# Kernel optimization log

Hardware: AMD Instinct MI355X
Metric: run time of the kernel (lower is better)

## Reference

```python
import jax, jax.numpy as jnp
import numpy as np

B, T, DQ, DV, A, F, K = 64, 1024, 1024, 512, 512, 32, 31


def setup_inputs() -> dict:
    key = jax.random.key(0)
    ks = jax.random.split(key, 8)
    query = jax.random.normal(ks[0], (B, DQ), jnp.float32)
    values = jax.random.normal(ks[1], (B, T, DV), jnp.float32)
    # decoder-step states (as produced by init_states)
    attention_cum = jnp.zeros((B, T), jnp.float32)
    attention_old = jnp.zeros((B, T), jnp.float32)
    alpha = jnp.concatenate([jnp.ones((B, 1), jnp.float32),
                             jnp.zeros((B, T - 1), jnp.float32) + 1e-7], axis=1)
    # learned parameters (Glorot-ish scaling)
    W_query = jax.random.normal(ks[2], (DQ, A), jnp.float32) / np.sqrt(DQ)
    W_inputs = jax.random.normal(ks[3], (DV, A), jnp.float32) / np.sqrt(DV)
    v_w = jax.random.normal(ks[4], (A, 1), jnp.float32) / np.sqrt(A)
    v_b = jnp.zeros((1,), jnp.float32)
    loc_kernel = jax.random.normal(ks[5], (K, 2, F), jnp.float32) / np.sqrt(K * 2)  # WIO
    W_loc = jax.random.normal(ks[6], (F, A), jnp.float32) / np.sqrt(F)
    return {"query": query, "values": values, "attention_cum": attention_cum,
            "attention_old": attention_old, "alpha": alpha,
            "W_query": W_query, "W_inputs": W_inputs, "v_w": v_w, "v_b": v_b,
            "loc_kernel": loc_kernel, "W_loc": W_loc}


def reference(query, values, attention_cum, attention_old, alpha,
              W_query, W_inputs, v_w, v_b, loc_kernel, W_loc):
    # process_values: cached projection of encoder memory  [B,T,A]
    processed_values = jnp.einsum('btd,da->bta', values, W_inputs)
    # location features: conv over stacked (old, cum) attention  [B,T,2]->[B,T,F]
    attn_cat = jnp.stack([attention_old, attention_cum], axis=2)
    conv = jax.lax.conv_general_dilated(attn_cat, loc_kernel, window_strides=(1,),
                                        padding='SAME',
                                        dimension_numbers=('NWC', 'WIO', 'NWC'))
    processed_attn = jnp.einsum('btf,fa->bta', conv, W_loc)
    # query projection  [B,1,A]
    processed_query = (query @ W_query)[:, None, :]
    # additive score  [B,T]
    score = (jnp.tanh(processed_values + processed_query + processed_attn) @ v_w)[..., 0] + v_b
    scores_norm = jax.nn.softmax(score, axis=-1)
    # forward attention recursion
    fwd_shifted = jnp.pad(alpha[:, :-1], ((0, 0), (1, 0)))
    new_alpha = (0.5 * alpha + 0.5 * fwd_shifted + 1e-8) * scores_norm
    new_alpha = new_alpha / jnp.sum(new_alpha, axis=1, keepdims=True)
    attn_weights = new_alpha
    # updated states
    new_cum = attention_cum + scores_norm
    new_old = attn_weights
    # context vector  [B,DV]
    context = jnp.einsum('bt,btd->bd', attn_weights, values)
    return (context, attn_weights, new_cum, new_old, new_alpha)
```

## Files before the change

### kernel.cpp

```cpp
#include <hip/hip_runtime.h>
#include <hip/hip_bf16.h>
#include <cstdint>
#include <cstddef>

#define B 64
#define T 1024
#define DQ 1024
#define DV 512
#define A_DIM 512
#define F_DIM 32
#define KW 31
#define M_TOT (B*T)
#define KEXT2 576
#define NCH 9

typedef __attribute__((ext_vector_type(8))) short short8;
typedef __attribute__((ext_vector_type(4))) float f32x4;
typedef __attribute__((ext_vector_type(4))) unsigned u32x4;

static __device__ __forceinline__ unsigned short f2bf(float f) {
    unsigned int u = __builtin_bit_cast(unsigned int, f);
    u += 0x7fffu + ((u >> 16) & 1u);
    return (unsigned short)(u >> 16);
}
static __device__ __forceinline__ float tanh_fast(float x) {
    float e = __expf(2.0f * x);
    return 1.0f - 2.0f * __builtin_amdgcn_rcpf(e + 1.0f);
}
static __device__ __forceinline__ short8 cvt8(f32x4 a, f32x4 b) {
    unsigned u0, u1, u2, u3;
    asm("v_cvt_pk_bf16_f32 %0, %1, %2" : "=v"(u0) : "v"(a[0]), "v"(a[1]));
    asm("v_cvt_pk_bf16_f32 %0, %1, %2" : "=v"(u1) : "v"(a[2]), "v"(a[3]));
    asm("v_cvt_pk_bf16_f32 %0, %1, %2" : "=v"(u2) : "v"(b[0]), "v"(b[1]));
    asm("v_cvt_pk_bf16_f32 %0, %1, %2" : "=v"(u3) : "v"(b[2]), "v"(b[3]));
    u32x4 u; u[0] = u0; u[1] = u1; u[2] = u2; u[3] = u3;
    return __builtin_bit_cast(short8, u);
}

#define LDSDMA16(gptr, lptr)                                                        \
    __builtin_amdgcn_global_load_lds(                                               \
        (const __attribute__((address_space(1))) void*)(const void*)(gptr),         \
        (__attribute__((address_space(3))) void*)(void*)(lptr), 16, 0, 0)

__global__ void prep_kernel(const float* __restrict__ query, const float* __restrict__ Wq,
                            const float* __restrict__ Wi, const float* __restrict__ Wl,
                            const float* __restrict__ old_, const float* __restrict__ cum_,
                            const float* __restrict__ lk,
                            float* __restrict__ pq,
                            float* __restrict__ score, unsigned short* __restrict__ Bt,
                            unsigned short* __restrict__ convb) {
    __shared__ __align__(16) char smem[16640];
    int bid = blockIdx.x, tid = threadIdx.x;
    if (bid < 512) {
        float (*red)[64] = (float(*)[64])smem;
        int pid = bid;
        int gid = pid * 256 + tid;
        if (gid < M_TOT) score[gid] = 0.f;
        int b = pid >> 3, a0 = (pid & 7) * 64;
        int al = tid & 63, ks = tid >> 6;
        const float* qr = query + (size_t)b * DQ + ks * 256;
        const float* wc = Wq + (size_t)(ks * 256) * A_DIM + a0 + al;
        float acc = 0.f;
        #pragma unroll 8
        for (int k = 0; k < 256; ++k) acc += qr[k] * wc[(size_t)k * A_DIM];
        red[ks][al] = acc;
        __syncthreads();
        if (ks == 0)
            pq[b * A_DIM + a0 + al] = red[0][al] + red[1][al] + red[2][al] + red[3][al];
    } else if (bid < 584) {
        float (*tile)[65] = (float(*)[65])smem;
        int tb = bid - 512;
        if (tb < 64) {
            int k0 = (tb >> 3) * 64, a0 = (tb & 7) * 64;
            int al = tid & 63, ko = tid >> 6;
            #pragma unroll
            for (int j = 0; j < 16; ++j) {
                int kl = j * 4 + ko;
                tile[kl][al] = Wi[(size_t)(k0 + kl) * A_DIM + a0 + al];
            }
            __syncthreads();
            int kl2 = tid & 63, ao = tid >> 6;
            #pragma unroll
            for (int j = 0; j < 16; ++j) {
                int al2 = j * 4 + ao;
                Bt[(size_t)(a0 + al2) * KEXT2 + k0 + kl2] = f2bf(tile[kl2][al2]);
            }
        } else {
            int a0 = (tb - 64) * 64;
            int al = tid & 63, ko = tid >> 6;
            #pragma unroll
            for (int j = 0; j < 8; ++j) {
                int kl = j * 4 + ko;
                tile[kl][al] = Wl[(size_t)kl * A_DIM + a0 + al];
            }
            __syncthreads();
            int kl2 = tid & 31, ao = tid >> 5;
            #pragma unroll
            for (int j = 0; j < 8; ++j) {
                int al2 = j * 8 + ao;
                Bt[(size_t)(a0 + al2) * KEXT2 + DV + kl2] = f2bf(tile[kl2][al2]);
            }
            #pragma unroll
            for (int j = 0; j < 8; ++j) {
                int idx = j * 256 + tid;
                int a_l = idx >> 5, kp = idx & 31;
                Bt[(size_t)(a0 + a_l) * KEXT2 + 544 + kp] = 0;
            }
        }
    } else {
        float* sOld = (float*)smem;
        float* sCum = sOld + 94;
        float* sLK  = sCum + 94;
        int cid = bid - 584;
        int b = cid >> 4, t0 = (cid & 15) * 64;
        int tl = tid & 63, fg = tid >> 6;
        for (int j = tid; j < 94; j += 256) {
            int tt = t0 - 15 + j;
            bool ok = (tt >= 0 && tt < T);
            sOld[j] = ok ? old_[b * T + tt] : 0.f;
            sCum[j] = ok ? cum_[b * T + tt] : 0.f;
        }
        for (int j = tid; j < KW * 2 * F_DIM; j += 256) sLK[j] = lk[j];
        __syncthreads();
        float acc[8];
        #pragma unroll
        for (int f = 0; f < 8; ++f) acc[f] = 0.f;
        for (int k = 0; k < KW; ++k) {
            float o = sOld[tl + k], c = sCum[tl + k];
            const float* lo = &sLK[(k * 2 + 0) * F_DIM + fg * 8];
            const float* lc = &sLK[(k * 2 + 1) * F_DIM + fg * 8];
            #pragma unroll
            for (int f = 0; f < 8; ++f) acc[f] += o * lo[f] + c * lc[f];
        }
        short8 pk;
        #pragma unroll
        for (int f = 0; f < 8; ++f) pk[f] = (short)f2bf(acc[f]);
        unsigned short* dst = convb + (size_t)(b * T + t0 + tl) * 64 + fg * 8;
        *(short8*)dst = pk;
        *(short8*)(dst + 32) = (short8)0;
    }
}

__launch_bounds__(256, 3)
__global__ void gemm_score(const float* __restrict__ values,
                           const unsigned short* __restrict__ Bt,
                           const unsigned short* __restrict__ convb,
                           const float* __restrict__ pq,
                           const float* __restrict__ vw,
                           float* __restrict__ score) {
    __shared__ __align__(16) float sAf[128 * 64];
    __shared__ __align__(16) short sB[128 * 64];
    __shared__ float sPQ[128];
    __shared__ float sVW[128];
    int tid = threadIdx.x;
    int x = blockIdx.x & 7, l = blockIdx.x >> 3;
    int mt = x * 64 + (l >> 2), nq = l & 3;
    int m0 = mt * 128, n0 = nq * 128;
    int b = m0 >> 10;
    if (tid < 128) { sPQ[tid] = pq[b * A_DIM + n0 + tid]; sVW[tid] = vw[n0 + tid]; }
    int w = tid >> 6, lane = tid & 63, q = lane >> 4, l15 = lane & 15;
    int wm = w & 1, wn = w >> 1;
    int trow = tid >> 4, pA = tid & 15;
    const float* aBase = values + (size_t)(m0 + trow) * DV + (pA ^ trow) * 4;
    int brow = tid >> 3, bseg = ((tid & 7) - brow) & 7;
    const unsigned short* bBase = Bt + (size_t)(n0 + brow) * KEXT2 + bseg * 8;
    const unsigned short* cBase = convb + (size_t)(m0 + brow) * 64 + bseg * 8;

    f32x4 acc[4][4];
    #pragma unroll
    for (int mi = 0; mi < 4; ++mi)
        #pragma unroll
        for (int ni = 0; ni < 4; ++ni) acc[mi][ni] = (f32x4)0.f;

    for (int c = 0; c < NCH; ++c) {
        __syncthreads();
        if (c < 8) {
            #pragma unroll
            for (int j = 0; j < 8; ++j)
                LDSDMA16(aBase + (size_t)j * 16 * DV + c * 64,
                         &sAf[(j * 256 + w * 64) * 4]);
        } else {
            #pragma unroll
            for (int j = 0; j < 4; ++j)
                LDSDMA16(cBase + j * 32 * 64,
                         (short*)sAf + (j * 256 + w * 64) * 8);
        }
        #pragma unroll
        for (int j = 0; j < 4; ++j)
            LDSDMA16(bBase + (size_t)j * 32 * KEXT2 + c * 64,
                     &sB[(j * 256 + w * 64) * 8]);
        __syncthreads();
        #pragma unroll
        for (int h = 0; h < 2; ++h) {
            short8 af[4], bfr[4];
            #pragma unroll
            for (int ni = 0; ni < 4; ++ni) {
                int r = wn * 64 + ni * 16 + l15;
                bfr[ni] = *(const short8*)&sB[r * 64 + ((((h * 4 + q) + r) & 7) << 3)];
            }
            if (c < 8) {
                #pragma unroll
                for (int mi = 0; mi < 4; ++mi) {
                    int r = wm * 64 + mi * 16 + l15;
                    int ps = (h * 8 + q * 2) ^ l15;
                    f32x4 lo = *(const f32x4*)&sAf[r * 64 + ps * 4];
                    f32x4 hi = *(const f32x4*)&sAf[r * 64 + (ps ^ 1) * 4];
                    af[mi] = cvt8(lo, hi);
                }
            } else {
                const short* sAh = (const short*)sAf;
                #pragma unroll
                for (int mi = 0; mi < 4; ++mi) {
                    int r = wm * 64 + mi * 16 + l15;
                    af[mi] = *(const short8*)&sAh[r * 64 + ((((h * 4 + q) + r) & 7) << 3)];
                }
            }
            #pragma unroll
            for (int mi = 0; mi < 4; ++mi)
                #pragma unroll
                for (int ni = 0; ni < 4; ++ni)
                    acc[mi][ni] = __builtin_amdgcn_mfma_f32_16x16x32_bf16(af[mi], bfr[ni], acc[mi][ni], 0, 0, 0);
        }
    }
    #pragma unroll
    for (int mi = 0; mi < 4; ++mi) {
        #pragma unroll
        for (int r = 0; r < 4; ++r) {
            float s = 0.f;
            #pragma unroll
            for (int ni = 0; ni < 4; ++ni) {
                int col = wn * 64 + ni * 16 + l15;
                float xv = acc[mi][ni][r] + sPQ[col];
                s += tanh_fast(xv) * sVW[col];
            }
            #pragma unroll
            for (int off = 1; off < 16; off <<= 1) s += __shfl_xor(s, off, 64);
            if (l15 == 0)
                atomicAdd(&score[m0 + wm * 64 + mi * 16 + q * 4 + r], s);
        }
    }
}

__global__ void softmax_fwd(const float* __restrict__ score,
                            const float* __restrict__ alpha,
                            const float* __restrict__ cum,
                            float* __restrict__ out) {
    int b = blockIdx.x, t = threadIdx.x;
    __shared__ float sred[16];
    __shared__ float sbc;
    float sc = score[b * T + t];
    int wid = t >> 6, lane = t & 63;
    float m = sc;
    #pragma unroll
    for (int off = 32; off; off >>= 1) m = fmaxf(m, __shfl_xor(m, off, 64));
    if (lane == 0) sred[wid] = m;
    __syncthreads();
    if (t == 0) { float mm = sred[0]; for (int i = 1; i < 16; ++i) mm = fmaxf(mm, sred[i]); sbc = mm; }
    __syncthreads();
    float M = sbc;
    float e = __expf(sc - M);
    float s = e;
    #pragma unroll
    for (int off = 32; off; off >>= 1) s += __shfl_xor(s, off, 64);
    __syncthreads();
    if (lane == 0) sred[wid] = s;
    __syncthreads();
    if (t == 0) { float ss = 0.f; for (int i = 0; i < 16; ++i) ss += sred[i]; sbc = ss; }
    __syncthreads();
    float sn = e / sbc;
    float a_t = alpha[b * T + t];
    float a_p = (t > 0) ? alpha[b * T + t - 1] : 0.f;
    float ua = (0.5f * (a_t + a_p) + 1e-8f) * sn;
    float u = ua;
    #pragma unroll
    for (int off = 32; off; off >>= 1) u += __shfl_xor(u, off, 64);
    __syncthreads();
    if (lane == 0) sred[wid] = u;
    __syncthreads();
    if (t == 0) { float ss = 0.f; for (int i = 0; i < 16; ++i) ss += sred[i]; sbc = ss; }
    __syncthreads();
    float wgt = ua / sbc;
    float* attnw  = out + B * DV;
    float* ncum   = attnw + B * T;
    float* nold   = ncum + B * T;
    float* nalpha = nold + B * T;
    attnw[b * T + t]  = wgt;
    ncum[b * T + t]   = cum[b * T + t] + sn;
    nold[b * T + t]   = wgt;
    nalpha[b * T + t] = wgt;
    if (t < DV) out[b * DV + t] = 0.f;
}

__global__ void context_kernel(const float* __restrict__ values,
                               float* __restrict__ out) {
    __shared__ float red[4][256];
    const float* attnw = out + B * DV;
    int b = blockIdx.x >> 5, tq = (blockIdx.x >> 1) & 15, dh = blockIdx.x & 1;
    int sub = threadIdx.x >> 6, dg = threadIdx.x & 63;
    int t0 = tq * 64 + sub * 16;
    int d0 = dh * 256 + dg * 4;
    float acc[4];
    #pragma unroll
    for (int f = 0; f < 4; ++f) acc[f] = 0.f;
    for (int tt = 0; tt < 16; ++tt) {
        int t = t0 + tt;
        float wgt = attnw[b * T + t];
        float4 xv = *(const float4*)(values + (size_t)(b * T + t) * DV + d0);
        acc[0] += wgt * xv.x; acc[1] += wgt * xv.y;
        acc[2] += wgt * xv.z; acc[3] += wgt * xv.w;
    }
    #pragma unroll
    for (int f = 0; f < 4; ++f) red[sub][dg * 4 + f] = acc[f];
    __syncthreads();
    if (sub == 0) {
        #pragma unroll
        for (int f = 0; f < 4; ++f) {
            int di = dg * 4 + f;
            float s = red[0][di] + red[1][di] + red[2][di] + red[3][di];
            atomicAdd(&out[b * DV + dh * 256 + di], s);
        }
    }
}

extern "C" void kernel_launch(void* const* d_in, const int* in_sizes, int n_in,
                              void* d_out, int out_size, void* d_ws, size_t ws_size,
                              hipStream_t stream) {
    const float* query  = (const float*)d_in[0];
    const float* values = (const float*)d_in[1];
    const float* cum    = (const float*)d_in[2];
    const float* old_   = (const float*)d_in[3];
    const float* alpha  = (const float*)d_in[4];
    const float* Wq     = (const float*)d_in[5];
    const float* Wi     = (const float*)d_in[6];
    const float* vw     = (const float*)d_in[7];
    const float* lk     = (const float*)d_in[9];
    const float* Wl     = (const float*)d_in[10];
    float* out = (float*)d_out;
    char* ws = (char*)d_ws;
    float* ws_pq            = (float*)(ws);
    float* ws_score         = (float*)(ws + 131072);
    unsigned short* ws_Bt   = (unsigned short*)(ws + 393216);
    unsigned short* ws_conv = (unsigned short*)(ws + 1048576);

    prep_kernel<<<1608, 256, 0, stream>>>(query, Wq, Wi, Wl, old_, cum, lk,
                                          ws_pq, ws_score, ws_Bt, ws_conv);
    gemm_score<<<2048, 256, 0, stream>>>(values, ws_Bt, ws_conv, ws_pq, vw, ws_score);
    softmax_fwd<<<64, 1024, 0, stream>>>(ws_score, alpha, cum, out);
    context_kernel<<<2048, 256, 0, stream>>>(values, out);
}
```

Measured before the change: 295.9 us.

## Double-buffer LDS in gemm_score and widen N tile to 256

```diff
diff --git a/kernel.cpp b/kernel.cpp
--- a/kernel.cpp
+++ b/kernel.cpp
@@ -141,27 +141,27 @@
     }
 }
 
-__launch_bounds__(256, 3)
+__launch_bounds__(512, 1)
 __global__ void gemm_score(const float* __restrict__ values,
                            const unsigned short* __restrict__ Bt,
                            const unsigned short* __restrict__ convb,
                            const float* __restrict__ pq,
                            const float* __restrict__ vw,
                            float* __restrict__ score) {
-    __shared__ __align__(16) float sAf[128 * 64];
-    __shared__ __align__(16) short sB[128 * 64];
-    __shared__ float sPQ[128];
-    __shared__ float sVW[128];
+    __shared__ __align__(16) float sAf[2][128 * 64];
+    __shared__ __align__(16) short sB[2][256 * 64];
+    __shared__ float sPQ[256];
+    __shared__ float sVW[256];
     int tid = threadIdx.x;
     int x = blockIdx.x & 7, l = blockIdx.x >> 3;
-    int mt = x * 64 + (l >> 2), nq = l & 3;
-    int m0 = mt * 128, n0 = nq * 128;
+    int mt = x * 64 + (l >> 1), nq = l & 1;
+    int m0 = mt * 128, n0 = nq * 256;
     int b = m0 >> 10;
-    if (tid < 128) { sPQ[tid] = pq[b * A_DIM + n0 + tid]; sVW[tid] = vw[n0 + tid]; }
+    if (tid < 256) { sPQ[tid] = pq[b * A_DIM + n0 + tid]; sVW[tid] = vw[n0 + tid]; }
     int w = tid >> 6, lane = tid & 63, q = lane >> 4, l15 = lane & 15;
     int wm = w & 1, wn = w >> 1;
     int trow = tid >> 4, pA = tid & 15;
-    const float* aBase = values + (size_t)(m0 + trow) * DV + (pA ^ trow) * 4;
+    const float* aBase = values + (size_t)(m0 + trow) * DV + ((pA ^ (trow & 15)) * 4);
     int brow = tid >> 3, bseg = ((tid & 7) - brow) & 7;
     const unsigned short* bBase = Bt + (size_t)(n0 + brow) * KEXT2 + bseg * 8;
     const unsigned short* cBase = convb + (size_t)(m0 + brow) * 64 + bseg * 8;
@@ -172,43 +172,53 @@
         #pragma unroll
         for (int ni = 0; ni < 4; ++ni) acc[mi][ni] = (f32x4)0.f;
 
+    #pragma unroll
+    for (int j = 0; j < 4; ++j)
+        LDSDMA16(aBase + (size_t)j * 32 * DV, &sAf[0][(j * 512 + w * 64) * 4]);
+    #pragma unroll
+    for (int j = 0; j < 4; ++j)
+        LDSDMA16(bBase + (size_t)j * 64 * KEXT2, &sB[0][(j * 512 + w * 64) * 8]);
+    __syncthreads();
+
+    int cur = 0;
     for (int c = 0; c < NCH; ++c) {
-        __syncthreads();
-        if (c < 8) {
-            #pragma unroll
-            for (int j = 0; j < 8; ++j)
-                LDSDMA16(aBase + (size_t)j * 16 * DV + c * 64,
-                         &sAf[(j * 256 + w * 64) * 4]);
-        } else {
+        int nxt = cur ^ 1;
+        if (c + 1 < NCH) {
+            if (c + 1 < 8) {
+                #pragma unroll
+                for (int j = 0; j < 4; ++j)
+                    LDSDMA16(aBase + (size_t)j * 32 * DV + (c + 1) * 64,
+                             &sAf[nxt][(j * 512 + w * 64) * 4]);
+            } else {
+                #pragma unroll
+                for (int j = 0; j < 2; ++j)
+                    LDSDMA16(cBase + j * 64 * 64,
+                             (short*)&sAf[nxt][0] + (j * 512 + w * 64) * 8);
+            }
             #pragma unroll
             for (int j = 0; j < 4; ++j)
-                LDSDMA16(cBase + j * 32 * 64,
-                         (short*)sAf + (j * 256 + w * 64) * 8);
-        }
-        #pragma unroll
-        for (int j = 0; j < 4; ++j)
-            LDSDMA16(bBase + (size_t)j * 32 * KEXT2 + c * 64,
-                     &sB[(j * 256 + w * 64) * 8]);
-        __syncthreads();
+                LDSDMA16(bBase + (size_t)j * 64 * KEXT2 + (c + 1) * 64,
+                         &sB[nxt][(j * 512 + w * 64) * 8]);
+        }
         #pragma unroll
         for (int h = 0; h < 2; ++h) {
             short8 af[4], bfr[4];
             #pragma unroll
             for (int ni = 0; ni < 4; ++ni) {
                 int r = wn * 64 + ni * 16 + l15;
-                bfr[ni] = *(const short8*)&sB[r * 64 + ((((h * 4 + q) + r) & 7) << 3)];
+                bfr[ni] = *(const short8*)&sB[cur][r * 64 + ((((h * 4 + q) + r) & 7) << 3)];
             }
             if (c < 8) {
                 #pragma unroll
                 for (int mi = 0; mi < 4; ++mi) {
                     int r = wm * 64 + mi * 16 + l15;
                     int ps = (h * 8 + q * 2) ^ l15;
-                    f32x4 lo = *(const f32x4*)&sAf[r * 64 + ps * 4];
-                    f32x4 hi = *(const f32x4*)&sAf[r * 64 + (ps ^ 1) * 4];
+                    f32x4 lo = *(const f32x4*)&sAf[cur][r * 64 + ps * 4];
+                    f32x4 hi = *(const f32x4*)&sAf[cur][r * 64 + (ps ^ 1) * 4];
                     af[mi] = cvt8(lo, hi);
                 }
             } else {
-                const short* sAh = (const short*)sAf;
+                const short* sAh = (const short*)&sAf[cur][0];
                 #pragma unroll
                 for (int mi = 0; mi < 4; ++mi) {
                     int r = wm * 64 + mi * 16 + l15;
@@ -221,6 +231,8 @@
                 for (int ni = 0; ni < 4; ++ni)
                     acc[mi][ni] = __builtin_amdgcn_mfma_f32_16x16x32_bf16(af[mi], bfr[ni], acc[mi][ni], 0, 0, 0);
         }
+        __syncthreads();
+        cur = nxt;
     }
     #pragma unroll
     for (int mi = 0; mi < 4; ++mi) {
@@ -344,7 +356,7 @@
 
     prep_kernel<<<1608, 256, 0, stream>>>(query, Wq, Wi, Wl, old_, cum, lk,
                                           ws_pq, ws_score, ws_Bt, ws_conv);
-    gemm_score<<<2048, 256, 0, stream>>>(values, ws_Bt, ws_conv, ws_pq, vw, ws_score);
+    gemm_score<<<1024, 512, 0, stream>>>(values, ws_Bt, ws_conv, ws_pq, vw, ws_score);
     softmax_fwd<<<64, 1024, 0, stream>>>(ws_score, alpha, cum, out);
     context_kernel<<<2048, 256, 0, stream>>>(values, out);
 }
```

After: 318.6 us. +7.7%, slower.

## Load GEMM operands directly from global into registers, dropping LDS staging

Applied to the files above, without the earlier changes.

```diff
diff --git a/kernel.cpp b/kernel.cpp
--- a/kernel.cpp
+++ b/kernel.cpp
@@ -12,7 +12,6 @@
 #define KW 31
 #define M_TOT (B*T)
 #define KEXT2 576
-#define NCH 9
 
 typedef __attribute__((ext_vector_type(8))) short short8;
 typedef __attribute__((ext_vector_type(4))) float f32x4;
@@ -36,11 +35,6 @@
     u32x4 u; u[0] = u0; u[1] = u1; u[2] = u2; u[3] = u3;
     return __builtin_bit_cast(short8, u);
 }
-
-#define LDSDMA16(gptr, lptr)                                                        \
-    __builtin_amdgcn_global_load_lds(                                               \
-        (const __attribute__((address_space(1))) void*)(const void*)(gptr),         \
-        (__attribute__((address_space(3))) void*)(void*)(lptr), 16, 0, 0)
 
 __global__ void prep_kernel(const float* __restrict__ query, const float* __restrict__ Wq,
                             const float* __restrict__ Wi, const float* __restrict__ Wl,
@@ -148,23 +142,23 @@
                            const float* __restrict__ pq,
                            const float* __restrict__ vw,
                            float* __restrict__ score) {
-    __shared__ __align__(16) float sAf[128 * 64];
-    __shared__ __align__(16) short sB[128 * 64];
-    __shared__ float sPQ[128];
-    __shared__ float sVW[128];
     int tid = threadIdx.x;
     int x = blockIdx.x & 7, l = blockIdx.x >> 3;
     int mt = x * 64 + (l >> 2), nq = l & 3;
     int m0 = mt * 128, n0 = nq * 128;
     int b = m0 >> 10;
-    if (tid < 128) { sPQ[tid] = pq[b * A_DIM + n0 + tid]; sVW[tid] = vw[n0 + tid]; }
     int w = tid >> 6, lane = tid & 63, q = lane >> 4, l15 = lane & 15;
     int wm = w & 1, wn = w >> 1;
-    int trow = tid >> 4, pA = tid & 15;
-    const float* aBase = values + (size_t)(m0 + trow) * DV + (pA ^ trow) * 4;
-    int brow = tid >> 3, bseg = ((tid & 7) - brow) & 7;
-    const unsigned short* bBase = Bt + (size_t)(n0 + brow) * KEXT2 + bseg * 8;
-    const unsigned short* cBase = convb + (size_t)(m0 + brow) * 64 + bseg * 8;
+    int arow = m0 + wm * 64 + l15;
+    int bcol = n0 + wn * 64 + l15;
+    const float* aP0 = values + (size_t)(arow +  0) * DV + q * 8;
+    const float* aP1 = values + (size_t)(arow + 16) * DV + q * 8;
+    const float* aP2 = values + (size_t)(arow + 32) * DV + q * 8;
+    const float* aP3 = values + (size_t)(arow + 48) * DV + q * 8;
+    const unsigned short* bP0 = Bt + (size_t)(bcol +  0) * KEXT2 + q * 8;
+    const unsigned short* bP1 = Bt + (size_t)(bcol + 16) * KEXT2 + q * 8;
+    const unsigned short* bP2 = Bt + (size_t)(bcol + 32) * KEXT2 + q * 8;
+    const unsigned short* bP3 = Bt + (size_t)(bcol + 48) * KEXT2 + q * 8;
 
     f32x4 acc[4][4];
     #pragma unroll
@@ -172,55 +166,54 @@
         #pragma unroll
         for (int ni = 0; ni < 4; ++ni) acc[mi][ni] = (f32x4)0.f;
 
-    for (int c = 0; c < NCH; ++c) {
-        __syncthreads();
-        if (c < 8) {
-            #pragma unroll
-            for (int j = 0; j < 8; ++j)
-                LDSDMA16(aBase + (size_t)j * 16 * DV + c * 64,
-                         &sAf[(j * 256 + w * 64) * 4]);
-        } else {
-            #pragma unroll
-            for (int j = 0; j < 4; ++j)
-                LDSDMA16(cBase + j * 32 * 64,
-                         (short*)sAf + (j * 256 + w * 64) * 8);
-        }
-        #pragma unroll
-        for (int j = 0; j < 4; ++j)
-            LDSDMA16(bBase + (size_t)j * 32 * KEXT2 + c * 64,
-                     &sB[(j * 256 + w * 64) * 8]);
-        __syncthreads();
+    #pragma unroll 1
+    for (int c = 0; c < 8; ++c) {
         #pragma unroll
         for (int h = 0; h < 2; ++h) {
-            short8 af[4], bfr[4];
-            #pragma unroll
-            for (int ni = 0; ni < 4; ++ni) {
-                int r = wn * 64 + ni * 16 + l15;
-                bfr[ni] = *(const short8*)&sB[r * 64 + ((((h * 4 + q) + r) & 7) << 3)];
-            }
-            if (c < 8) {
-                #pragma unroll
-                for (int mi = 0; mi < 4; ++mi) {
-                    int r = wm * 64 + mi * 16 + l15;
-                    int ps = (h * 8 + q * 2) ^ l15;
-                    f32x4 lo = *(const f32x4*)&sAf[r * 64 + ps * 4];
-                    f32x4 hi = *(const f32x4*)&sAf[r * 64 + (ps ^ 1) * 4];
-                    af[mi] = cvt8(lo, hi);
-                }
-            } else {
-                const short* sAh = (const short*)sAf;
-                #pragma unroll
-                for (int mi = 0; mi < 4; ++mi) {
-                    int r = wm * 64 + mi * 16 + l15;
-                    af[mi] = *(const short8*)&sAh[r * 64 + ((((h * 4 + q) + r) & 7) << 3)];
-                }
-            }
+            f32x4 lo[4], hi[4];
+            short8 bfr[4], af[4];
+            lo[0] = *(const f32x4*)(aP0 + h * 32); hi[0] = *(const f32x4*)(aP0 + h * 32 + 4);
+            lo[1] = *(const f32x4*)(aP1 + h * 32); hi[1] = *(const f32x4*)(aP1 + h * 32 + 4);
+            lo[2] = *(const f32x4*)(aP2 + h * 32); hi[2] = *(const f32x4*)(aP2 + h * 32 + 4);
+            lo[3] = *(const f32x4*)(aP3 + h * 32); hi[3] = *(const f32x4*)(aP3 + h * 32 + 4);
+            bfr[0] = *(const short8*)(bP0 + h * 32);
+            bfr[1] = *(const short8*)(bP1 + h * 32);
+            bfr[2] = *(const short8*)(bP2 + h * 32);
+            bfr[3] = *(const short8*)(bP3 + h * 32);
+            #pragma unroll
+            for (int mi = 0; mi < 4; ++mi) af[mi] = cvt8(lo[mi], hi[mi]);
             #pragma unroll
             for (int mi = 0; mi < 4; ++mi)
                 #pragma unroll
                 for (int ni = 0; ni < 4; ++ni)
                     acc[mi][ni] = __builtin_amdgcn_mfma_f32_16x16x32_bf16(af[mi], bfr[ni], acc[mi][ni], 0, 0, 0);
         }
+        aP0 += 64; aP1 += 64; aP2 += 64; aP3 += 64;
+        bP0 += 64; bP1 += 64; bP2 += 64; bP3 += 64;
+    }
+    {
+        short8 af[4], bfr[4];
+        const unsigned short* cP = convb + (size_t)arow * 64 + q * 8;
+        af[0] = *(const short8*)(cP);
+        af[1] = *(const short8*)(cP + 16 * 64);
+        af[2] = *(const short8*)(cP + 32 * 64);
+        af[3] = *(const short8*)(cP + 48 * 64);
+        bfr[0] = *(const short8*)(bP0);
+        bfr[1] = *(const short8*)(bP1);
+        bfr[2] = *(const short8*)(bP2);
+        bfr[3] = *(const short8*)(bP3);
+        #pragma unroll
+        for (int mi = 0; mi < 4; ++mi)
+            #pragma unroll
+            for (int ni = 0; ni < 4; ++ni)
+                acc[mi][ni] = __builtin_amdgcn_mfma_f32_16x16x32_bf16(af[mi], bfr[ni], acc[mi][ni], 0, 0, 0);
+    }
+    float pqv[4], vwv[4];
+    #pragma unroll
+    for (int ni = 0; ni < 4; ++ni) {
+        int col = n0 + wn * 64 + ni * 16 + l15;
+        pqv[ni] = pq[b * A_DIM + col];
+        vwv[ni] = vw[col];
     }
     #pragma unroll
     for (int mi = 0; mi < 4; ++mi) {
@@ -229,9 +222,8 @@
             float s = 0.f;
             #pragma unroll
             for (int ni = 0; ni < 4; ++ni) {
-                int col = wn * 64 + ni * 16 + l15;
-                float xv = acc[mi][ni][r] + sPQ[col];
-                s += tanh_fast(xv) * sVW[col];
+                float xv = acc[mi][ni][r] + pqv[ni];
+                s += tanh_fast(xv) * vwv[ni];
             }
             #pragma unroll
             for (int off = 1; off < 16; off <<= 1) s += __shfl_xor(s, off, 64);
```

Result: slower. 406.7 us (+37.4%).

## Prefetch A via registers with bf16 LDS staging and double-buffer B in score GEMM

Applied to the files above, without the earlier changes.

```diff
diff --git a/kernel.cpp b/kernel.cpp
--- a/kernel.cpp
+++ b/kernel.cpp
@@ -12,7 +12,6 @@
 #define KW 31
 #define M_TOT (B*T)
 #define KEXT2 576
-#define NCH 9
 
 typedef __attribute__((ext_vector_type(8))) short short8;
 typedef __attribute__((ext_vector_type(4))) float f32x4;
@@ -148,8 +147,8 @@
                            const float* __restrict__ pq,
                            const float* __restrict__ vw,
                            float* __restrict__ score) {
-    __shared__ __align__(16) float sAf[128 * 64];
-    __shared__ __align__(16) short sB[128 * 64];
+    __shared__ __align__(16) short sA[128 * 64];
+    __shared__ __align__(16) short sB[2][128 * 64];
     __shared__ float sPQ[128];
     __shared__ float sVW[128];
     int tid = threadIdx.x;
@@ -160,11 +159,12 @@
     if (tid < 128) { sPQ[tid] = pq[b * A_DIM + n0 + tid]; sVW[tid] = vw[n0 + tid]; }
     int w = tid >> 6, lane = tid & 63, q = lane >> 4, l15 = lane & 15;
     int wm = w & 1, wn = w >> 1;
-    int trow = tid >> 4, pA = tid & 15;
-    const float* aBase = values + (size_t)(m0 + trow) * DV + (pA ^ trow) * 4;
-    int brow = tid >> 3, bseg = ((tid & 7) - brow) & 7;
-    const unsigned short* bBase = Bt + (size_t)(n0 + brow) * KEXT2 + bseg * 8;
-    const unsigned short* cBase = convb + (size_t)(m0 + brow) * 64 + bseg * 8;
+    int srow = tid >> 3, sseg = ((tid & 7) - srow) & 7;
+    const float* aSrc[4];
+    #pragma unroll
+    for (int j = 0; j < 4; ++j)
+        aSrc[j] = values + (size_t)(m0 + j * 32 + srow) * DV + sseg * 8;
+    const unsigned short* bBase = Bt + (size_t)(n0 + srow) * KEXT2 + sseg * 8;
 
     f32x4 acc[4][4];
     #pragma unroll
@@ -172,54 +172,82 @@
         #pragma unroll
         for (int ni = 0; ni < 4; ++ni) acc[mi][ni] = (f32x4)0.f;
 
-    for (int c = 0; c < NCH; ++c) {
-        __syncthreads();
-        if (c < 8) {
-            #pragma unroll
-            for (int j = 0; j < 8; ++j)
-                LDSDMA16(aBase + (size_t)j * 16 * DV + c * 64,
-                         &sAf[(j * 256 + w * 64) * 4]);
-        } else {
+    {
+        f32x4 plo[4], phi[4];
+        #pragma unroll
+        for (int j = 0; j < 4; ++j) {
+            plo[j] = *(const f32x4*)(aSrc[j]);
+            phi[j] = *(const f32x4*)(aSrc[j] + 4);
+        }
+        #pragma unroll
+        for (int j = 0; j < 4; ++j)
+            LDSDMA16(bBase + (size_t)j * 32 * KEXT2, &sB[0][(j * 256 + w * 64) * 8]);
+        #pragma unroll
+        for (int j = 0; j < 4; ++j)
+            *(short8*)&sA[(j * 256 + tid) * 8] = cvt8(plo[j], phi[j]);
+    }
+    __syncthreads();
+
+    #pragma unroll 1
+    for (int c = 0; c <= 8; ++c) {
+        int nxt = c + 1;
+        f32x4 lo4[4], hi4[4];
+        short8 cv[4];
+        if (nxt < 8) {
+            #pragma unroll
+            for (int j = 0; j < 4; ++j) {
+                lo4[j] = *(const f32x4*)(aSrc[j] + nxt * 64);
+                hi4[j] = *(const f32x4*)(aSrc[j] + nxt * 64 + 4);
+            }
             #pragma unroll
             for (int j = 0; j < 4; ++j)
-                LDSDMA16(cBase + j * 32 * 64,
-                         (short*)sAf + (j * 256 + w * 64) * 8);
-        }
-        #pragma unroll
-        for (int j = 0; j < 4; ++j)
-            LDSDMA16(bBase + (size_t)j * 32 * KEXT2 + c * 64,
-                     &sB[(j * 256 + w * 64) * 8]);
-        __syncthreads();
+                LDSDMA16(bBase + (size_t)j * 32 * KEXT2 + nxt * 64,
+                         &sB[nxt & 1][(j * 256 + w * 64) * 8]);
+        } else if (nxt == 8) {
+            #pragma unroll
+            for (int j = 0; j < 4; ++j)
+                cv[j] = *(const short8*)(convb + (size_t)(m0 + j * 32 + srow) * 64 + sseg * 8);
+            #pragma unroll
+            for (int j = 0; j < 4; ++j)
+                LDSDMA16(bBase + (size_t)j * 32 * KEXT2 + 8 * 64,
+                         &sB[0][(j * 256 + w * 64) * 8]);
+        }
         #pragma unroll
         for (int h = 0; h < 2; ++h) {
             short8 af[4], bfr[4];
+            int sgl = h * 4 + q;
+            #pragma unroll
+            for (int mi = 0; mi < 4; ++mi) {
+                int r = wm * 64 + mi * 16 + l15;
+                af[mi] = *(const short8*)&sA[r * 64 + (((sgl + r) & 7) << 3)];
+            }
             #pragma unroll
             for (int ni = 0; ni < 4; ++ni) {
                 int r = wn * 64 + ni * 16 + l15;
-                bfr[ni] = *(const short8*)&sB[r * 64 + ((((h * 4 + q) + r) & 7) << 3)];
-            }
-            if (c < 8) {
-                #pragma unroll
-                for (int mi = 0; mi < 4; ++mi) {
-                    int r = wm * 64 + mi * 16 + l15;
-                    int ps = (h * 8 + q * 2) ^ l15;
-                    f32x4 lo = *(const f32x4*)&sAf[r * 64 + ps * 4];
-                    f32x4 hi = *(const f32x4*)&sAf[r * 64 + (ps ^ 1) * 4];
-                    af[mi] = cvt8(lo, hi);
-                }
-            } else {
-                const short* sAh = (const short*)sAf;
-                #pragma unroll
-                for (int mi = 0; mi < 4; ++mi) {
-                    int r = wm * 64 + mi * 16 + l15;
-                    af[mi] = *(const short8*)&sAh[r * 64 + ((((h * 4 + q) + r) & 7) << 3)];
-                }
+                bfr[ni] = *(const short8*)&sB[c & 1][r * 64 + (((sgl + r) & 7) << 3)];
             }
             #pragma unroll
             for (int mi = 0; mi < 4; ++mi)
                 #pragma unroll
                 for (int ni = 0; ni < 4; ++ni)
                     acc[mi][ni] = __builtin_amdgcn_mfma_f32_16x16x32_bf16(af[mi], bfr[ni], acc[mi][ni], 0, 0, 0);
+        }
+        if (nxt <= 8) {
+            asm volatile("s_waitcnt lgkmcnt(0)" ::: "memory");
+            __builtin_amdgcn_s_barrier();
+            __builtin_amdgcn_sched_barrier(0);
+            short8 pk[4];
+            if (nxt < 8) {
+                #pragma unroll
+                for (int j = 0; j < 4; ++j) pk[j] = cvt8(lo4[j], hi4[j]);
+            } else {
+                #pragma unroll
+                for (int j = 0; j < 4; ++j) pk[j] = cv[j];
+            }
+            #pragma unroll
+            for (int j = 0; j < 4; ++j)
+                *(short8*)&sA[(j * 256 + tid) * 8] = pk[j];
+            __syncthreads();
         }
     }
     #pragma unroll
```

Measured after the change: 316.9 us. 1.07x slower.
